# Optimization experiments

Hardware: AMD Instinct MI355X
Metric: run time of the kernel (lower is better)

The kernel has to match this reference:

```python
import jax, jax.numpy as jnp
import numpy as np


def setup_inputs() -> dict:
    key = jax.random.key(0)
    C, S, NQ, H = 10, 10, 30, 1024  # n_classes, n_support, n_query, h_dim
    ks = jax.random.split(key, 6)
    x = jax.random.normal(ks[0], (C * (S + NQ), H), dtype=jnp.float32)
    # sorted, balanced labels so y.eq(c).nonzero() picks contiguous blocks
    y = jnp.repeat(jnp.arange(C, dtype=jnp.int32), S + NQ)
    W1 = jax.random.normal(ks[1], (H, H), dtype=jnp.float32) / np.sqrt(H)
    b1 = jnp.zeros((H,), dtype=jnp.float32)
    W2 = jax.random.normal(ks[2], (4 * H, H), dtype=jnp.float32) / np.sqrt(4 * H)
    b2 = jnp.zeros((H,), dtype=jnp.float32)
    return {"x": x, "W1": W1, "b1": b1, "W2": W2, "b2": b2,
            "y": y, "n_classes": C, "n_support": S, "n_query": NQ, "flag": 0}


def reference(x, W1, b1, W2, b2, y, n_classes, n_support, n_query, flag):
    # flag == 0 path; y is sorted & balanced, so the label-based gather in the
    # original (y.eq(c).nonzero()[:S] / [S:]) reduces to a reshape.
    C, S, NQ = n_classes, n_support, n_query
    H = x.shape[-1]
    xr = x.reshape(C, S + NQ, H)
    support = xr[:, :S]                      # [C, S, H]
    query = xr[:, S:].reshape(C * NQ, H)     # [Qt, H], Qt = C*NQ

    # fc1 computed ONCE on support/query, then broadcast (same math as
    # applying fc1 to the expanded tensors in the original).
    sf = jnp.einsum('csh,hd->csd', support, W1) + b1   # [C, S, H]
    qf = query @ W1 + b1                               # [Qt, H]

    # fc2 on concat([sf, qf, |sf-qf|, sf*qf]) split into 4 blocks of W2 so we
    # never materialize the [Qt, C, S, 4H] concat.
    Ws, Wq, Wc, Wd = W2[:H], W2[H:2 * H], W2[2 * H:3 * H], W2[3 * H:]
    a_s = jnp.einsum('csh,hd->csd', sf, Ws)            # [C, S, H]
    a_q = qf @ Wq                                      # [Qt, H]
    sfb = sf[None]                                     # [1, C, S, H]
    qfb = qf[:, None, None]                            # [Qt, 1, 1, H]
    d1 = jnp.abs(sfb - qfb)                            # [Qt, C, S, H]
    d2 = sfb * qfb                                     # [Qt, C, S, H]
    mca_ = (a_s[None] + a_q[:, None, None]
            + jnp.einsum('qcsh,hd->qcsd', d1, Wc)
            + jnp.einsum('qcsh,hd->qcsd', d2, Wd) + b2)  # [Qt, C, S, H]

    score = jax.nn.softmax(jnp.tanh(mca_).sum(-1), axis=-1)  # [Qt, C, S]
    proto = jnp.einsum('qcs,csh->qch', score, support)       # [Qt, C, H]
    dists = jnp.sum((proto - query[:, None, :]) ** 2, axis=-1)  # [Qt, C]
    return dists
```

## Files before the change

kernel.cpp:

```cpp
#include <hip/hip_runtime.h>
#include <hip/hip_bf16.h>
#include <math.h>

#define C_   10
#define S_   10
#define NQ_  30
#define H_   1024
#define Q_   300
#define ROWS_ 400

typedef __attribute__((ext_vector_type(8))) short s16x8;
typedef __attribute__((ext_vector_type(4))) float f32x4;

static __device__ __forceinline__ short f2b(float f) {
  __hip_bfloat16 h = __float2bfloat16(f);
  return __builtin_bit_cast(short, h);
}

static __device__ __forceinline__ float ftanh(float v) {
  v = fminf(fmaxf(v, -10.f), 10.f);
  float e = __expf(2.f * v);
  return (e - 1.f) / (e + 1.f);
}

__global__ __launch_bounds__(256) void feat_kernel(
    const float* __restrict__ x, const float* __restrict__ W1,
    const float* __restrict__ b1, float* __restrict__ f) {
  __shared__ float xs[4][H_];
  const int rt = blockIdx.x % 100;
  const int nt = blockIdx.x / 100;
  const int r0 = rt * 4;
  const int n0 = nt * 256;
  const int tid = threadIdx.x;

  for (int t = tid; t < 4 * H_ / 4; t += 256) {
    int r = t >> 8, h4 = (t & 255) * 4;
    *(float4*)&xs[r][h4] = *(const float4*)&x[(size_t)(r0 + r) * H_ + h4];
  }
  __syncthreads();

  float acc0 = 0.f, acc1 = 0.f, acc2 = 0.f, acc3 = 0.f;
  const float* __restrict__ wp = W1 + n0 + tid;
#pragma unroll 8
  for (int h = 0; h < H_; ++h) {
    float w = wp[(size_t)h * H_];
    acc0 = fmaf(xs[0][h], w, acc0);
    acc1 = fmaf(xs[1][h], w, acc1);
    acc2 = fmaf(xs[2][h], w, acc2);
    acc3 = fmaf(xs[3][h], w, acc3);
  }
  const int col = n0 + tid;
  const float bb = b1[col];
  f[(size_t)(r0 + 0) * H_ + col] = acc0 + bb;
  f[(size_t)(r0 + 1) * H_ + col] = acc1 + bb;
  f[(size_t)(r0 + 2) * H_ + col] = acc2 + bb;
  f[(size_t)(r0 + 3) * H_ + col] = acc3 + bb;
}

__global__ __launch_bounds__(256) void proj_kernel(
    const float* __restrict__ f, const float* __restrict__ W2,
    const float* __restrict__ b2, float* __restrict__ a) {
  __shared__ float fs[4][H_];
  const int rt = blockIdx.x % 100;
  const int nt = blockIdx.x / 100;
  const bool isSup = (rt < 25);
  const int i0 = isSup ? rt * 4 : (rt - 25) * 4;
  const int n0 = nt * 256;
  const float* __restrict__ W = isSup ? W2 : (W2 + (size_t)H_ * H_);
  const int tid = threadIdx.x;

  for (int t = tid; t < 4 * H_ / 4; t += 256) {
    int r = t >> 8, h4 = (t & 255) * 4;
    int i = i0 + r;
    int row = isSup ? ((i / 10) * 40 + (i % 10)) : ((i / 30) * 40 + 10 + (i % 30));
    *(float4*)&fs[r][h4] = *(const float4*)&f[(size_t)row * H_ + h4];
  }
  __syncthreads();

  float acc0 = 0.f, acc1 = 0.f, acc2 = 0.f, acc3 = 0.f;
  const float* __restrict__ wp = W + n0 + tid;
#pragma unroll 8
  for (int h = 0; h < H_; ++h) {
    float w = wp[(size_t)h * H_];
    acc0 = fmaf(fs[0][h], w, acc0);
    acc1 = fmaf(fs[1][h], w, acc1);
    acc2 = fmaf(fs[2][h], w, acc2);
    acc3 = fmaf(fs[3][h], w, acc3);
  }
  const int col = n0 + tid;
  const float bb = isSup ? 0.f : b2[col];
  const int o0 = isSup ? i0 : (100 + i0);
  a[(size_t)(o0 + 0) * H_ + col] = acc0 + bb;
  a[(size_t)(o0 + 1) * H_ + col] = acc1 + bb;
  a[(size_t)(o0 + 2) * H_ + col] = acc2 + bb;
  a[(size_t)(o0 + 3) * H_ + col] = acc3 + bb;
}

__global__ __launch_bounds__(256) void trans_kernel(
    const float* __restrict__ W2, unsigned short* __restrict__ Bt,
    float* __restrict__ logits) {
  const int b = blockIdx.x;
  const int tid = threadIdx.x;
  if (b == 512) {
    float4* lz = (float4*)logits;
    for (int i = tid; i < 7500; i += 256) lz[i] = make_float4(0.f, 0.f, 0.f, 0.f);
    return;
  }
  const int mat = b >> 8, kt = (b >> 4) & 15, ntl = b & 15;
  const float* __restrict__ src =
      W2 + (size_t)(2 + mat) * H_ * H_ + (size_t)(kt * 64) * H_ + ntl * 64;
  __shared__ float tl[64][65];
  {
    int r = tid >> 2, c4 = (tid & 3) * 16;
    const float* srcp = src + (size_t)r * H_ + c4;
#pragma unroll
    for (int j = 0; j < 4; ++j) {
      float4 v = *(const float4*)(srcp + j * 4);
      tl[r][c4 + j * 4 + 0] = v.x;
      tl[r][c4 + j * 4 + 1] = v.y;
      tl[r][c4 + j * 4 + 2] = v.z;
      tl[r][c4 + j * 4 + 3] = v.w;
    }
  }
  __syncthreads();
  {
    int n = tid >> 2, k0t = (tid & 3) * 16;
    s16x8 o0, o1;
#pragma unroll
    for (int j = 0; j < 8; ++j) {
      o0[j] = f2b(tl[k0t + j][n]);
      o1[j] = f2b(tl[k0t + 8 + j][n]);
    }
    unsigned short* dstp = Bt + (size_t)mat * H_ * H_ +
                           (size_t)(ntl * 64 + n) * H_ + kt * 64 + k0t;
    *(s16x8*)dstp = o0;
    *(s16x8*)(dstp + 8) = o1;
  }
}

__global__ __launch_bounds__(256, 2) void mca_mfma_kernel(
    const float* __restrict__ f, const float* __restrict__ a,
    const unsigned short* __restrict__ Bt, float* __restrict__ logits) {
  const int b = blockIdx.x;
  const int nt = b & 7;
  const int qt = (b >> 3) % 19;
  const int c = (b >> 3) / 19;
  const int q0 = qt * 16;
  const int n0 = nt * 128;

  __shared__ unsigned short Bls[2][128 * 64];
  __shared__ float sl[2][26][36];

  const int tid = threadIdx.x;
  const int w = tid >> 6, lane = tid & 63;
  const int frow = lane & 15;
  const int lq = lane >> 4;
  const int wr = w >> 1, wc = w & 1;

  const int str = tid >> 3, sseg = tid & 7;
  int sgrow;
  if (str < 10) sgrow = c * 40 + str;
  else {
    int qg = q0 + (str - 10);
    if (qg > 299) qg = 299;
    sgrow = (qg / 30) * 40 + 10 + (qg % 30);
  }
  const float* fb_stage = f + (size_t)sgrow * H_ + sseg * 4;
  const unsigned st_off = (unsigned)(str * 144 + sseg * 16);

  const unsigned qfo = (unsigned)((10 + frow) * 144 + lq * 32);
  unsigned sfo[5];
#pragma unroll
  for (int m = 0; m < 5; ++m) sfo[m] = (unsigned)((wr * 5 + m) * 144 + lq * 32);

  const int rlo = lane >> 3;
  const int cch = (lane & 7) ^ rlo;
  const unsigned short* bsrc[4];
  unsigned bldso[4];
#pragma unroll
  for (int i = 0; i < 4; ++i) {
    int row = w * 32 + i * 8 + rlo;
    bsrc[i] = Bt + (size_t)(cch >> 2) * H_ * H_ + (size_t)(n0 + row) * H_ +
              (cch & 3) * 8;
    bldso[i] = (unsigned)(w * 4096 + i * 1024);
  }

  const unsigned fkb = (unsigned)(lq * 16);
  const unsigned swf = (unsigned)((frow & 7) << 4);
  unsigned brd[4];
#pragma unroll
  for (int nf = 0; nf < 4; ++nf) brd[nf] = (unsigned)((wc * 64 + nf * 16 + frow) * 128);

  f32x4 acc[5][4];
#pragma unroll
  for (int m = 0; m < 5; ++m)
#pragma unroll
    for (int nf = 0; nf < 4; ++nf) acc[m][nf] = (f32x4)(0.f);

#define STAGE(SLP, KS)                                                         \
  do {                                                                         \
    if (tid < 208) {                                                           \
      float4 v = *(const float4*)(fb_stage + (KS) * 32);                       \
      *(float4*)((char*)&sl[SLP][0][0] + st_off) = v;                          \
    }                                                                          \
  } while (0)

#define DMA_B(P, KG)                                                           \
  do {                                                                         \
    _Pragma("unroll") for (int i = 0; i < 4; ++i) {                            \
      __builtin_amdgcn_global_load_lds(                                        \
          (const __attribute__((address_space(1))) unsigned int*)(bsrc[i] + (KG)), \
          (__attribute__((address_space(3))) unsigned int*)((char*)&Bls[P][0] + bldso[i]), \
          16, 0, 0);                                                           \
    }                                                                          \
  } while (0)

#define STEP_BODY(P)                                                           \
  do {                                                                         \
    const char* SLB = (const char*)&sl[P][0][0];                               \
    const char* BB = (const char*)&Bls[P][0];                                  \
    float4 qa = *(const float4*)(SLB + qfo);                                   \
    float4 qb = *(const float4*)(SLB + qfo + 16);                              \
    s16x8 bf0 = *(const s16x8*)(BB + ((brd[0] + fkb) ^ swf));                  \
    s16x8 bf1 = *(const s16x8*)(BB + ((brd[1] + fkb) ^ swf));                  \
    s16x8 bf2 = *(const s16x8*)(BB + ((brd[2] + fkb) ^ swf));                  \
    s16x8 bf3 = *(const s16x8*)(BB + ((brd[3] + fkb) ^ swf));                  \
    s16x8 bg0 = *(const s16x8*)(BB + ((brd[0] + fkb + 64) ^ swf));             \
    s16x8 bg1 = *(const s16x8*)(BB + ((brd[1] + fkb + 64) ^ swf));             \
    s16x8 bg2 = *(const s16x8*)(BB + ((brd[2] + fkb + 64) ^ swf));             \
    s16x8 bg3 = *(const s16x8*)(BB + ((brd[3] + fkb + 64) ^ swf));             \
    __builtin_amdgcn_s_setprio(1);                                            \
    _Pragma("unroll") for (int m = 0; m < 5; ++m) {                            \
      float4 sa = *(const float4*)(SLB + sfo[m]);                              \
      float4 sb = *(const float4*)(SLB + sfo[m] + 16);                         \
      s16x8 t1, t2;                                                            \
      t1[0] = f2b(fabsf(sa.x - qa.x)); t2[0] = f2b(sa.x * qa.x);               \
      t1[1] = f2b(fabsf(sa.y - qa.y)); t2[1] = f2b(sa.y * qa.y);               \
      t1[2] = f2b(fabsf(sa.z - qa.z)); t2[2] = f2b(sa.z * qa.z);               \
      t1[3] = f2b(fabsf(sa.w - qa.w)); t2[3] = f2b(sa.w * qa.w);               \
      t1[4] = f2b(fabsf(sb.x - qb.x)); t2[4] = f2b(sb.x * qb.x);               \
      t1[5] = f2b(fabsf(sb.y - qb.y)); t2[5] = f2b(sb.y * qb.y);               \
      t1[6] = f2b(fabsf(sb.z - qb.z)); t2[6] = f2b(sb.z * qb.z);               \
      t1[7] = f2b(fabsf(sb.w - qb.w)); t2[7] = f2b(sb.w * qb.w);               \
      acc[m][0] = __builtin_amdgcn_mfma_f32_16x16x32_bf16(t1, bf0, acc[m][0], 0, 0, 0); \
      acc[m][1] = __builtin_amdgcn_mfma_f32_16x16x32_bf16(t1, bf1, acc[m][1], 0, 0, 0); \
      acc[m][2] = __builtin_amdgcn_mfma_f32_16x16x32_bf16(t1, bf2, acc[m][2], 0, 0, 0); \
      acc[m][3] = __builtin_amdgcn_mfma_f32_16x16x32_bf16(t1, bf3, acc[m][3], 0, 0, 0); \
      acc[m][0] = __builtin_amdgcn_mfma_f32_16x16x32_bf16(t2, bg0, acc[m][0], 0, 0, 0); \
      acc[m][1] = __builtin_amdgcn_mfma_f32_16x16x32_bf16(t2, bg1, acc[m][1], 0, 0, 0); \
      acc[m][2] = __builtin_amdgcn_mfma_f32_16x16x32_bf16(t2, bg2, acc[m][2], 0, 0, 0); \
      acc[m][3] = __builtin_amdgcn_mfma_f32_16x16x32_bf16(t2, bg3, acc[m][3], 0, 0, 0); \
    }                                                                          \
    __builtin_amdgcn_s_setprio(0);                                            \
  } while (0)

  STAGE(0, 0);
  DMA_B(0, 0);
  __syncthreads();

  for (int kp = 0; kp < 16; ++kp) {
    const int ks = kp * 2;
    DMA_B(1, (ks + 1) * 32);
    STAGE(1, ks + 1);
    STEP_BODY(0);
    __syncthreads();
    if (kp < 15) {
      DMA_B(0, (ks + 2) * 32);
      STAGE(0, ks + 2);
      STEP_BODY(1);
      __syncthreads();
    } else {
      STEP_BODY(1);
    }
  }

  const int colb = n0 + wc * 64 + frow;
  const int rgrp = lq * 4;
#pragma unroll
  for (int m = 0; m < 5; ++m) {
    const int s = wr * 5 + m;
#pragma unroll
    for (int r = 0; r < 4; ++r) {
      const int q = q0 + rgrp + r;
      float t = 0.f;
#pragma unroll
      for (int nf = 0; nf < 4; ++nf) {
        const int col = colb + nf * 16;
        float v = acc[m][nf][r] + a[(size_t)(c * 10 + s) * H_ + col] +
                  a[(size_t)(100 + (q < 300 ? q : 299)) * H_ + col];
        t += ftanh(v);
      }
      t += __shfl_xor(t, 1);
      t += __shfl_xor(t, 2);
      t += __shfl_xor(t, 4);
      t += __shfl_xor(t, 8);
      if ((lane & 15) == 0 && q < 300)
        atomicAdd(&logits[(q * 10 + c) * 10 + s], t);
    }
  }
#undef STAGE
#undef DMA_B
#undef STEP_BODY
}

__global__ __launch_bounds__(256) void out_kernel(
    const float* __restrict__ x, const float* __restrict__ logits,
    float* __restrict__ dists) {
  const int q = blockIdx.x / 10;
  const int c = blockIdx.x % 10;
  const int tid = threadIdx.x;
  const int lane = tid & 63;
  const int wave = tid >> 6;
  __shared__ float red[4];

  float l[S_];
  float m = -1e30f;
#pragma unroll
  for (int s = 0; s < S_; ++s) {
    l[s] = logits[(q * 10 + c) * 10 + s];
    m = fmaxf(m, l[s]);
  }
  float sum = 0.f;
  float sc[S_];
#pragma unroll
  for (int s = 0; s < S_; ++s) {
    sc[s] = __expf(l[s] - m);
    sum += sc[s];
  }
  float inv = 1.f / sum;
#pragma unroll
  for (int s = 0; s < S_; ++s) sc[s] *= inv;

  const int qr = (q / 30) * 40 + 10 + (q % 30);
  float part = 0.f;
#pragma unroll
  for (int ii = 0; ii < 4; ++ii) {
    int i = tid + ii * 256;
    float p = 0.f;
#pragma unroll
    for (int s = 0; s < S_; ++s)
      p = fmaf(sc[s], x[(size_t)(c * 40 + s) * H_ + i], p);
    float d = p - x[(size_t)qr * H_ + i];
    part = fmaf(d, d, part);
  }
  for (int off = 32; off; off >>= 1) part += __shfl_down(part, off);
  if (lane == 0) red[wave] = part;
  __syncthreads();
  if (tid == 0) dists[q * 10 + c] = red[0] + red[1] + red[2] + red[3];
}

extern "C" void kernel_launch(void* const* d_in, const int* in_sizes, int n_in,
                              void* d_out, int out_size, void* d_ws, size_t ws_size,
                              hipStream_t stream) {
  const float* x = (const float*)d_in[0];
  const float* W1 = (const float*)d_in[1];
  const float* b1 = (const float*)d_in[2];
  const float* W2 = (const float*)d_in[3];
  const float* b2 = (const float*)d_in[4];
  float* out = (float*)d_out;

  float* f = (float*)d_ws;
  float* a = f + ROWS_ * H_;
  float* logits = a + ROWS_ * H_;
  unsigned short* Bt = (unsigned short*)(logits + 30208);

  feat_kernel<<<400, 256, 0, stream>>>(x, W1, b1, f);
  proj_kernel<<<400, 256, 0, stream>>>(f, W2, b2, a);
  trans_kernel<<<513, 256, 0, stream>>>(W2, Bt, logits);
  mca_mfma_kernel<<<10 * 19 * 8, 256, 0, stream>>>(f, a, Bt, logits);
  out_kernel<<<3000, 256, 0, stream>>>(x, logits, out);
}
```

Before: 300.6 us.

## Widen MCA MFMA N-tile to 256 columns and reorder loop around B fragments

Each block of the MCA kernel now covers 256 output columns instead of 128, so the grid halves to 760 blocks and every staged support/query tile is reused across twice as many columns. The inner loop is reordered: the five |s-q| fragments (then the five s*q fragments) are built first, and each B fragment read from LDS feeds five MFMAs. This cuts repeated generation of the elementwise operands and B LDS reads per MFMA. In exchange the accumulator doubles to 160 floats per thread and LDS use grows to about 64KB per block, which risks register spills and lower occupancy, and the smaller grid may underfill the 256 CUs.

```diff
diff --git a/kernel.cpp b/kernel.cpp
--- a/kernel.cpp
+++ b/kernel.cpp
@@ -142,13 +142,13 @@
     const float* __restrict__ f, const float* __restrict__ a,
     const unsigned short* __restrict__ Bt, float* __restrict__ logits) {
   const int b = blockIdx.x;
-  const int nt = b & 7;
-  const int qt = (b >> 3) % 19;
-  const int c = (b >> 3) / 19;
+  const int nt = b & 3;
+  const int qt = (b >> 2) % 19;
+  const int c = (b >> 2) / 19;
   const int q0 = qt * 16;
-  const int n0 = nt * 128;
-
-  __shared__ unsigned short Bls[2][128 * 64];
+  const int n0 = nt * 256;
+
+  __shared__ unsigned short Bls[2][256 * 64];
   __shared__ float sl[2][26][36];
 
   const int tid = threadIdx.x;
@@ -169,33 +169,22 @@
   const unsigned st_off = (unsigned)(str * 144 + sseg * 16);
 
   const unsigned qfo = (unsigned)((10 + frow) * 144 + lq * 32);
-  unsigned sfo[5];
-#pragma unroll
-  for (int m = 0; m < 5; ++m) sfo[m] = (unsigned)((wr * 5 + m) * 144 + lq * 32);
+  const unsigned sfo0 = (unsigned)((wr * 5) * 144 + lq * 32);
 
   const int rlo = lane >> 3;
   const int cch = (lane & 7) ^ rlo;
-  const unsigned short* bsrc[4];
-  unsigned bldso[4];
-#pragma unroll
-  for (int i = 0; i < 4; ++i) {
-    int row = w * 32 + i * 8 + rlo;
-    bsrc[i] = Bt + (size_t)(cch >> 2) * H_ * H_ + (size_t)(n0 + row) * H_ +
-              (cch & 3) * 8;
-    bldso[i] = (unsigned)(w * 4096 + i * 1024);
-  }
+  const unsigned short* bsrc0 = Bt + (size_t)(cch >> 2) * H_ * H_ +
+                                (size_t)(n0 + w * 64 + rlo) * H_ + (cch & 3) * 8;
 
   const unsigned fkb = (unsigned)(lq * 16);
   const unsigned swf = (unsigned)((frow & 7) << 4);
-  unsigned brd[4];
-#pragma unroll
-  for (int nf = 0; nf < 4; ++nf) brd[nf] = (unsigned)((wc * 64 + nf * 16 + frow) * 128);
-
-  f32x4 acc[5][4];
+  const unsigned brd0 = (unsigned)((wc * 128 + frow) * 128);
+
+  f32x4 acc[5][8];
 #pragma unroll
   for (int m = 0; m < 5; ++m)
 #pragma unroll
-    for (int nf = 0; nf < 4; ++nf) acc[m][nf] = (f32x4)(0.f);
+    for (int nf = 0; nf < 8; ++nf) acc[m][nf] = (f32x4)(0.f);
 
 #define STAGE(SLP, KS)                                                         \
   do {                                                                         \
@@ -207,11 +196,52 @@
 
 #define DMA_B(P, KG)                                                           \
   do {                                                                         \
-    _Pragma("unroll") for (int i = 0; i < 4; ++i) {                            \
+    _Pragma("unroll") for (int i = 0; i < 8; ++i) {                            \
       __builtin_amdgcn_global_load_lds(                                        \
-          (const __attribute__((address_space(1))) unsigned int*)(bsrc[i] + (KG)), \
-          (__attribute__((address_space(3))) unsigned int*)((char*)&Bls[P][0] + bldso[i]), \
+          (const __attribute__((address_space(1))) unsigned int*)(bsrc0 +      \
+              (size_t)i * 8 * H_ + (KG)),                                      \
+          (__attribute__((address_space(3))) unsigned int*)((char*)&Bls[P][0] + \
+              (w * 8192 + i * 1024)),                                          \
           16, 0, 0);                                                           \
+    }                                                                          \
+  } while (0)
+
+#define GEN_D1(MM, TT)                                                         \
+  do {                                                                         \
+    float4 sa = *(const float4*)(SLB + sfo0 + (MM) * 144);                     \
+    float4 sb = *(const float4*)(SLB + sfo0 + (MM) * 144 + 16);                \
+    s16x8 tt;                                                                  \
+    tt[0] = f2b(fabsf(sa.x - qa.x)); tt[1] = f2b(fabsf(sa.y - qa.y));          \
+    tt[2] = f2b(fabsf(sa.z - qa.z)); tt[3] = f2b(fabsf(sa.w - qa.w));          \
+    tt[4] = f2b(fabsf(sb.x - qb.x)); tt[5] = f2b(fabsf(sb.y - qb.y));          \
+    tt[6] = f2b(fabsf(sb.z - qb.z)); tt[7] = f2b(fabsf(sb.w - qb.w));          \
+    TT = tt;                                                                   \
+  } while (0)
+
+#define GEN_D2(MM, TT)                                                         \
+  do {                                                                         \
+    float4 sa = *(const float4*)(SLB + sfo0 + (MM) * 144);                     \
+    float4 sb = *(const float4*)(SLB + sfo0 + (MM) * 144 + 16);                \
+    s16x8 tt;                                                                  \
+    tt[0] = f2b(sa.x * qa.x); tt[1] = f2b(sa.y * qa.y);                        \
+    tt[2] = f2b(sa.z * qa.z); tt[3] = f2b(sa.w * qa.w);                        \
+    tt[4] = f2b(sb.x * qb.x); tt[5] = f2b(sb.y * qb.y);                        \
+    tt[6] = f2b(sb.z * qb.z); tt[7] = f2b(sb.w * qb.w);                        \
+    TT = tt;                                                                   \
+  } while (0)
+
+#define BREAD(NF, KOFF)                                                        \
+  (*(const s16x8*)(BB + ((brd0 + (NF) * 2048 + fkb + (KOFF)) ^ swf)))
+
+#define MFMA_ROW(TT0, TT1, TT2, TT3, TT4, KOFF)                                \
+  do {                                                                         \
+    _Pragma("unroll") for (int nf = 0; nf < 8; ++nf) {                         \
+      s16x8 bfr = BREAD(nf, KOFF);                                             \
+      acc[0][nf] = __builtin_amdgcn_mfma_f32_16x16x32_bf16(TT0, bfr, acc[0][nf], 0, 0, 0); \
+      acc[1][nf] = __builtin_amdgcn_mfma_f32_16x16x32_bf16(TT1, bfr, acc[1][nf], 0, 0, 0); \
+      acc[2][nf] = __builtin_amdgcn_mfma_f32_16x16x32_bf16(TT2, bfr, acc[2][nf], 0, 0, 0); \
+      acc[3][nf] = __builtin_amdgcn_mfma_f32_16x16x32_bf16(TT3, bfr, acc[3][nf], 0, 0, 0); \
+      acc[4][nf] = __builtin_amdgcn_mfma_f32_16x16x32_bf16(TT4, bfr, acc[4][nf], 0, 0, 0); \
     }                                                                          \
   } while (0)
 
@@ -221,36 +251,14 @@
     const char* BB = (const char*)&Bls[P][0];                                  \
     float4 qa = *(const float4*)(SLB + qfo);                                   \
     float4 qb = *(const float4*)(SLB + qfo + 16);                              \
-    s16x8 bf0 = *(const s16x8*)(BB + ((brd[0] + fkb) ^ swf));                  \
-    s16x8 bf1 = *(const s16x8*)(BB + ((brd[1] + fkb) ^ swf));                  \
-    s16x8 bf2 = *(const s16x8*)(BB + ((brd[2] + fkb) ^ swf));                  \
-    s16x8 bf3 = *(const s16x8*)(BB + ((brd[3] + fkb) ^ swf));                  \
-    s16x8 bg0 = *(const s16x8*)(BB + ((brd[0] + fkb + 64) ^ swf));             \
-    s16x8 bg1 = *(const s16x8*)(BB + ((brd[1] + fkb + 64) ^ swf));             \
-    s16x8 bg2 = *(const s16x8*)(BB + ((brd[2] + fkb + 64) ^ swf));             \
-    s16x8 bg3 = *(const s16x8*)(BB + ((brd[3] + fkb + 64) ^ swf));             \
+    s16x8 t0, t1, t2, t3, t4;                                                  \
+    GEN_D1(0, t0); GEN_D1(1, t1); GEN_D1(2, t2); GEN_D1(3, t3); GEN_D1(4, t4); \
     __builtin_amdgcn_s_setprio(1);                                            \
-    _Pragma("unroll") for (int m = 0; m < 5; ++m) {                            \
-      float4 sa = *(const float4*)(SLB + sfo[m]);                              \
-      float4 sb = *(const float4*)(SLB + sfo[m] + 16);                         \
-      s16x8 t1, t2;                                                            \
-      t1[0] = f2b(fabsf(sa.x - qa.x)); t2[0] = f2b(sa.x * qa.x);               \
-      t1[1] = f2b(fabsf(sa.y - qa.y)); t2[1] = f2b(sa.y * qa.y);               \
-      t1[2] = f2b(fabsf(sa.z - qa.z)); t2[2] = f2b(sa.z * qa.z);               \
-      t1[3] = f2b(fabsf(sa.w - qa.w)); t2[3] = f2b(sa.w * qa.w);               \
-      t1[4] = f2b(fabsf(sb.x - qb.x)); t2[4] = f2b(sb.x * qb.x);               \
-      t1[5] = f2b(fabsf(sb.y - qb.y)); t2[5] = f2b(sb.y * qb.y);               \
-      t1[6] = f2b(fabsf(sb.z - qb.z)); t2[6] = f2b(sb.z * qb.z);               \
-      t1[7] = f2b(fabsf(sb.w - qb.w)); t2[7] = f2b(sb.w * qb.w);               \
-      acc[m][0] = __builtin_amdgcn_mfma_f32_16x16x32_bf16(t1, bf0, acc[m][0], 0, 0, 0); \
-      acc[m][1] = __builtin_amdgcn_mfma_f32_16x16x32_bf16(t1, bf1, acc[m][1], 0, 0, 0); \
-      acc[m][2] = __builtin_amdgcn_mfma_f32_16x16x32_bf16(t1, bf2, acc[m][2], 0, 0, 0); \
-      acc[m][3] = __builtin_amdgcn_mfma_f32_16x16x32_bf16(t1, bf3, acc[m][3], 0, 0, 0); \
-      acc[m][0] = __builtin_amdgcn_mfma_f32_16x16x32_bf16(t2, bg0, acc[m][0], 0, 0, 0); \
-      acc[m][1] = __builtin_amdgcn_mfma_f32_16x16x32_bf16(t2, bg1, acc[m][1], 0, 0, 0); \
-      acc[m][2] = __builtin_amdgcn_mfma_f32_16x16x32_bf16(t2, bg2, acc[m][2], 0, 0, 0); \
-      acc[m][3] = __builtin_amdgcn_mfma_f32_16x16x32_bf16(t2, bg3, acc[m][3], 0, 0, 0); \
-    }                                                                          \
+    MFMA_ROW(t0, t1, t2, t3, t4, 0);                                           \
+    __builtin_amdgcn_s_setprio(0);                                            \
+    GEN_D2(0, t0); GEN_D2(1, t1); GEN_D2(2, t2); GEN_D2(3, t3); GEN_D2(4, t4); \
+    __builtin_amdgcn_s_setprio(1);                                            \
+    MFMA_ROW(t0, t1, t2, t3, t4, 64);                                          \
     __builtin_amdgcn_s_setprio(0);                                            \
   } while (0)
 
@@ -274,7 +282,7 @@
     }
   }
 
-  const int colb = n0 + wc * 64 + frow;
+  const int colb = n0 + wc * 128 + frow;
   const int rgrp = lq * 4;
 #pragma unroll
   for (int m = 0; m < 5; ++m) {
@@ -284,7 +292,7 @@
       const int q = q0 + rgrp + r;
       float t = 0.f;
 #pragma unroll
-      for (int nf = 0; nf < 4; ++nf) {
+      for (int nf = 0; nf < 8; ++nf) {
         const int col = colb + nf * 16;
         float v = acc[m][nf][r] + a[(size_t)(c * 10 + s) * H_ + col] +
                   a[(size_t)(100 + (q < 300 ? q : 299)) * H_ + col];
@@ -300,6 +308,10 @@
   }
 #undef STAGE
 #undef DMA_B
+#undef GEN_D1
+#undef GEN_D2
+#undef BREAD
+#undef MFMA_ROW
 #undef STEP_BODY
 }
 
@@ -367,6 +379,6 @@
   feat_kernel<<<400, 256, 0, stream>>>(x, W1, b1, f);
   proj_kernel<<<400, 256, 0, stream>>>(f, W2, b2, a);
   trans_kernel<<<513, 256, 0, stream>>>(W2, Bt, logits);
-  mca_mfma_kernel<<<10 * 19 * 8, 256, 0, stream>>>(f, a, Bt, logits);
+  mca_mfma_kernel<<<10 * 19 * 4, 256, 0, stream>>>(f, a, Bt, logits);
   out_kernel<<<3000, 256, 0, stream>>>(x, logits, out);
 }
```

Result: slower. 1.192 ms (+296.7%).

## Drop LDS staging in MCA kernel, load operands directly from global memory

Applied to the files above, without the earlier changes.

Removes the double-buffered LDS staging of support/query features and the async global-to-LDS DMA of the bf16 weight tiles. Each wave now reads its MFMA operands straight from global memory (relying on cache), with a simple unrolled k-loop and no block barriers. Occupancy hint is raised from 2 to 3 blocks per CU. This trades LDS traffic and sync for redundant global/L2 loads across waves and less explicit latency hiding.

```diff
diff --git a/kernel.cpp b/kernel.cpp
--- a/kernel.cpp
+++ b/kernel.cpp
@@ -138,7 +138,7 @@
   }
 }
 
-__global__ __launch_bounds__(256, 2) void mca_mfma_kernel(
+__global__ __launch_bounds__(256, 3) void mca_mfma_kernel(
     const float* __restrict__ f, const float* __restrict__ a,
     const unsigned short* __restrict__ Bt, float* __restrict__ logits) {
   const int b = blockIdx.x;
@@ -148,48 +148,30 @@
   const int q0 = qt * 16;
   const int n0 = nt * 128;
 
-  __shared__ unsigned short Bls[2][128 * 64];
-  __shared__ float sl[2][26][36];
-
   const int tid = threadIdx.x;
   const int w = tid >> 6, lane = tid & 63;
   const int frow = lane & 15;
   const int lq = lane >> 4;
   const int wr = w >> 1, wc = w & 1;
 
-  const int str = tid >> 3, sseg = tid & 7;
-  int sgrow;
-  if (str < 10) sgrow = c * 40 + str;
-  else {
-    int qg = q0 + (str - 10);
-    if (qg > 299) qg = 299;
-    sgrow = (qg / 30) * 40 + 10 + (qg % 30);
-  }
-  const float* fb_stage = f + (size_t)sgrow * H_ + sseg * 4;
-  const unsigned st_off = (unsigned)(str * 144 + sseg * 16);
-
-  const unsigned qfo = (unsigned)((10 + frow) * 144 + lq * 32);
-  unsigned sfo[5];
-#pragma unroll
-  for (int m = 0; m < 5; ++m) sfo[m] = (unsigned)((wr * 5 + m) * 144 + lq * 32);
-
-  const int rlo = lane >> 3;
-  const int cch = (lane & 7) ^ rlo;
-  const unsigned short* bsrc[4];
-  unsigned bldso[4];
-#pragma unroll
-  for (int i = 0; i < 4; ++i) {
-    int row = w * 32 + i * 8 + rlo;
-    bsrc[i] = Bt + (size_t)(cch >> 2) * H_ * H_ + (size_t)(n0 + row) * H_ +
-              (cch & 3) * 8;
-    bldso[i] = (unsigned)(w * 4096 + i * 1024);
-  }
-
-  const unsigned fkb = (unsigned)(lq * 16);
-  const unsigned swf = (unsigned)((frow & 7) << 4);
-  unsigned brd[4];
-#pragma unroll
-  for (int nf = 0; nf < 4; ++nf) brd[nf] = (unsigned)((wc * 64 + nf * 16 + frow) * 128);
+  int qg = q0 + frow;
+  if (qg > 299) qg = 299;
+  const float* __restrict__ qfp =
+      f + (size_t)((qg / 30) * 40 + 10 + (qg % 30)) * H_ + lq * 8;
+
+  const float* __restrict__ sfp[5];
+#pragma unroll
+  for (int m = 0; m < 5; ++m)
+    sfp[m] = f + (size_t)(c * 40 + wr * 5 + m) * H_ + lq * 8;
+
+  const unsigned short* __restrict__ bcp[4];
+  const unsigned short* __restrict__ bdp[4];
+#pragma unroll
+  for (int nf = 0; nf < 4; ++nf) {
+    size_t row = (size_t)(n0 + wc * 64 + nf * 16 + frow);
+    bcp[nf] = Bt + row * H_ + lq * 8;
+    bdp[nf] = Bt + (size_t)H_ * H_ + row * H_ + lq * 8;
+  }
 
   f32x4 acc[5][4];
 #pragma unroll
@@ -197,81 +179,45 @@
 #pragma unroll
     for (int nf = 0; nf < 4; ++nf) acc[m][nf] = (f32x4)(0.f);
 
-#define STAGE(SLP, KS)                                                         \
-  do {                                                                         \
-    if (tid < 208) {                                                           \
-      float4 v = *(const float4*)(fb_stage + (KS) * 32);                       \
-      *(float4*)((char*)&sl[SLP][0][0] + st_off) = v;                          \
-    }                                                                          \
-  } while (0)
-
-#define DMA_B(P, KG)                                                           \
-  do {                                                                         \
-    _Pragma("unroll") for (int i = 0; i < 4; ++i) {                            \
-      __builtin_amdgcn_global_load_lds(                                        \
-          (const __attribute__((address_space(1))) unsigned int*)(bsrc[i] + (KG)), \
-          (__attribute__((address_space(3))) unsigned int*)((char*)&Bls[P][0] + bldso[i]), \
-          16, 0, 0);                                                           \
-    }                                                                          \
-  } while (0)
-
-#define STEP_BODY(P)                                                           \
-  do {                                                                         \
-    const char* SLB = (const char*)&sl[P][0][0];                               \
-    const char* BB = (const char*)&Bls[P][0];                                  \
-    float4 qa = *(const float4*)(SLB + qfo);                                   \
-    float4 qb = *(const float4*)(SLB + qfo + 16);                              \
-    s16x8 bf0 = *(const s16x8*)(BB + ((brd[0] + fkb) ^ swf));                  \
-    s16x8 bf1 = *(const s16x8*)(BB + ((brd[1] + fkb) ^ swf));                  \
-    s16x8 bf2 = *(const s16x8*)(BB + ((brd[2] + fkb) ^ swf));                  \
-    s16x8 bf3 = *(const s16x8*)(BB + ((brd[3] + fkb) ^ swf));                  \
-    s16x8 bg0 = *(const s16x8*)(BB + ((brd[0] + fkb + 64) ^ swf));             \
-    s16x8 bg1 = *(const s16x8*)(BB + ((brd[1] + fkb + 64) ^ swf));             \
-    s16x8 bg2 = *(const s16x8*)(BB + ((brd[2] + fkb + 64) ^ swf));             \
-    s16x8 bg3 = *(const s16x8*)(BB + ((brd[3] + fkb + 64) ^ swf));             \
-    __builtin_amdgcn_s_setprio(1);                                            \
-    _Pragma("unroll") for (int m = 0; m < 5; ++m) {                            \
-      float4 sa = *(const float4*)(SLB + sfo[m]);                              \
-      float4 sb = *(const float4*)(SLB + sfo[m] + 16);                         \
-      s16x8 t1, t2;                                                            \
-      t1[0] = f2b(fabsf(sa.x - qa.x)); t2[0] = f2b(sa.x * qa.x);               \
-      t1[1] = f2b(fabsf(sa.y - qa.y)); t2[1] = f2b(sa.y * qa.y);               \
-      t1[2] = f2b(fabsf(sa.z - qa.z)); t2[2] = f2b(sa.z * qa.z);               \
-      t1[3] = f2b(fabsf(sa.w - qa.w)); t2[3] = f2b(sa.w * qa.w);               \
-      t1[4] = f2b(fabsf(sb.x - qb.x)); t2[4] = f2b(sb.x * qb.x);               \
-      t1[5] = f2b(fabsf(sb.y - qb.y)); t2[5] = f2b(sb.y * qb.y);               \
-      t1[6] = f2b(fabsf(sb.z - qb.z)); t2[6] = f2b(sb.z * qb.z);               \
-      t1[7] = f2b(fabsf(sb.w - qb.w)); t2[7] = f2b(sb.w * qb.w);               \
-      acc[m][0] = __builtin_amdgcn_mfma_f32_16x16x32_bf16(t1, bf0, acc[m][0], 0, 0, 0); \
-      acc[m][1] = __builtin_amdgcn_mfma_f32_16x16x32_bf16(t1, bf1, acc[m][1], 0, 0, 0); \
-      acc[m][2] = __builtin_amdgcn_mfma_f32_16x16x32_bf16(t1, bf2, acc[m][2], 0, 0, 0); \
-      acc[m][3] = __builtin_amdgcn_mfma_f32_16x16x32_bf16(t1, bf3, acc[m][3], 0, 0, 0); \
-      acc[m][0] = __builtin_amdgcn_mfma_f32_16x16x32_bf16(t2, bg0, acc[m][0], 0, 0, 0); \
-      acc[m][1] = __builtin_amdgcn_mfma_f32_16x16x32_bf16(t2, bg1, acc[m][1], 0, 0, 0); \
-      acc[m][2] = __builtin_amdgcn_mfma_f32_16x16x32_bf16(t2, bg2, acc[m][2], 0, 0, 0); \
-      acc[m][3] = __builtin_amdgcn_mfma_f32_16x16x32_bf16(t2, bg3, acc[m][3], 0, 0, 0); \
-    }                                                                          \
-    __builtin_amdgcn_s_setprio(0);                                            \
-  } while (0)
-
-  STAGE(0, 0);
-  DMA_B(0, 0);
-  __syncthreads();
-
-  for (int kp = 0; kp < 16; ++kp) {
-    const int ks = kp * 2;
-    DMA_B(1, (ks + 1) * 32);
-    STAGE(1, ks + 1);
-    STEP_BODY(0);
-    __syncthreads();
-    if (kp < 15) {
-      DMA_B(0, (ks + 2) * 32);
-      STAGE(0, ks + 2);
-      STEP_BODY(1);
-      __syncthreads();
-    } else {
-      STEP_BODY(1);
+#pragma unroll 2
+  for (int ks = 0; ks < 32; ++ks) {
+    const int ko = ks * 32;
+
+    float4 qa = *(const float4*)(qfp + ko);
+    float4 qb = *(const float4*)(qfp + ko + 4);
+    s16x8 bf0 = *(const s16x8*)(bcp[0] + ko);
+    s16x8 bf1 = *(const s16x8*)(bcp[1] + ko);
+    s16x8 bf2 = *(const s16x8*)(bcp[2] + ko);
+    s16x8 bf3 = *(const s16x8*)(bcp[3] + ko);
+    s16x8 bg0 = *(const s16x8*)(bdp[0] + ko);
+    s16x8 bg1 = *(const s16x8*)(bdp[1] + ko);
+    s16x8 bg2 = *(const s16x8*)(bdp[2] + ko);
+    s16x8 bg3 = *(const s16x8*)(bdp[3] + ko);
+
+    __builtin_amdgcn_s_setprio(1);
+#pragma unroll
+    for (int m = 0; m < 5; ++m) {
+      float4 sa = *(const float4*)(sfp[m] + ko);
+      float4 sb = *(const float4*)(sfp[m] + ko + 4);
+      s16x8 t1, t2;
+      t1[0] = f2b(fabsf(sa.x - qa.x)); t2[0] = f2b(sa.x * qa.x);
+      t1[1] = f2b(fabsf(sa.y - qa.y)); t2[1] = f2b(sa.y * qa.y);
+      t1[2] = f2b(fabsf(sa.z - qa.z)); t2[2] = f2b(sa.z * qa.z);
+      t1[3] = f2b(fabsf(sa.w - qa.w)); t2[3] = f2b(sa.w * qa.w);
+      t1[4] = f2b(fabsf(sb.x - qb.x)); t2[4] = f2b(sb.x * qb.x);
+      t1[5] = f2b(fabsf(sb.y - qb.y)); t2[5] = f2b(sb.y * qb.y);
+      t1[6] = f2b(fabsf(sb.z - qb.z)); t2[6] = f2b(sb.z * qb.z);
+      t1[7] = f2b(fabsf(sb.w - qb.w)); t2[7] = f2b(sb.w * qb.w);
+      acc[m][0] = __builtin_amdgcn_mfma_f32_16x16x32_bf16(t1, bf0, acc[m][0], 0, 0, 0);
+      acc[m][1] = __builtin_amdgcn_mfma_f32_16x16x32_bf16(t1, bf1, acc[m][1], 0, 0, 0);
+      acc[m][2] = __builtin_amdgcn_mfma_f32_16x16x32_bf16(t1, bf2, acc[m][2], 0, 0, 0);
+      acc[m][3] = __builtin_amdgcn_mfma_f32_16x16x32_bf16(t1, bf3, acc[m][3], 0, 0, 0);
+      acc[m][0] = __builtin_amdgcn_mfma_f32_16x16x32_bf16(t2, bg0, acc[m][0], 0, 0, 0);
+      acc[m][1] = __builtin_amdgcn_mfma_f32_16x16x32_bf16(t2, bg1, acc[m][1], 0, 0, 0);
+      acc[m][2] = __builtin_amdgcn_mfma_f32_16x16x32_bf16(t2, bg2, acc[m][2], 0, 0, 0);
+      acc[m][3] = __builtin_amdgcn_mfma_f32_16x16x32_bf16(t2, bg3, acc[m][3], 0, 0, 0);
     }
+    __builtin_amdgcn_s_setprio(0);
   }
 
   const int colb = n0 + wc * 64 + frow;
@@ -298,9 +244,6 @@
         atomicAdd(&logits[(q * 10 + c) * 10 + s], t);
     }
   }
-#undef STAGE
-#undef DMA_B
-#undef STEP_BODY
 }
 
 __global__ __launch_bounds__(256) void out_kernel(
```

After: 465.0 us. 1.55x slower.
